# Kernel optimization log

Measured on AMD Instinct MI355X. Metric: run time of the kernel, lower is better.

Reference implementation:

```python
import jax, jax.numpy as jnp
import numpy as np

B, C, H, W = 4, 512, 32, 32
NUM_HEADS, DIM_HEAD = 16, 32
DIM_ATTN = NUM_HEADS * DIM_HEAD  # 512
N = H * W


def setup_inputs() -> dict:
    key = jax.random.key(0)
    ks = jax.random.split(key, 6)
    s = 0.02
    return {
        "x": jax.random.normal(ks[0], (B, C, H, W), jnp.float32),
        "w_qkv": jax.random.normal(ks[1], (3 * DIM_ATTN, C), jnp.float32) * s,
        "b_qkv": jax.random.normal(ks[2], (3 * DIM_ATTN,), jnp.float32) * s,
        "w_proj": jax.random.normal(ks[3], (C, DIM_ATTN), jnp.float32) * s,
        "b_proj": jax.random.normal(ks[4], (C,), jnp.float32) * s,
        "shared_rel_pos": jax.random.normal(ks[5], (1, NUM_HEADS, N, N), jnp.float32) * s,
    }


def reference(x, w_qkv, b_qkv, w_proj, b_proj, shared_rel_pos):
    b, c, h, w = x.shape
    n = h * w
    scale = DIM_HEAD ** -0.5
    # 1x1 conv == per-pixel matmul over channels
    qkv = jnp.einsum('bchw,oc->bohw', x, w_qkv) + b_qkv[None, :, None, None]
    # [B, heads, 3*dh, N] -> chunk along dim 2 (matches torch .chunk(3, dim=2))
    qkv = qkv.reshape(b, NUM_HEADS, 3 * DIM_HEAD, n)
    q, k, v = jnp.split(qkv, 3, axis=2)          # each [B, heads, dh, N]
    attn = jnp.einsum('bhdi,bhdj->bhij', q, k) * scale  # q^T @ k
    attn = attn + shared_rel_pos
    attn = jax.nn.softmax(attn, axis=-1)
    out = jnp.einsum('bhdj,bhij->bhdi', v, attn)  # v @ attn^T, [B, heads, dh, N]
    out = out.reshape(b, NUM_HEADS * DIM_HEAD, h, w)
    out = jnp.einsum('bchw,oc->bohw', out, w_proj) + b_proj[None, :, None, None]
    return out
```

## Files before the change

kernel.cpp:

```cpp
#include <hip/hip_runtime.h>
#include <cstdint>
#include <cstddef>

#define BATCH 4
#define CIN   512
#define NPIX  1024
#define HEADS 16
#define DH    32
#define DATTN 512
#define O_QKV 1536

typedef unsigned short u16;
typedef __bf16 bf16x4 __attribute__((ext_vector_type(4)));
typedef __bf16 bf16x8 __attribute__((ext_vector_type(8)));
typedef float  f32x4  __attribute__((ext_vector_type(4)));

typedef const __attribute__((address_space(1))) void g1_t;
typedef __attribute__((address_space(3))) void l3_t;

#if defined(__has_builtin)
#if __has_builtin(__builtin_amdgcn_exp2f)
#define EXP2(x) __builtin_amdgcn_exp2f(x)
#endif
#endif
#ifndef EXP2
#define EXP2(x) __expf((x) * 0.6931471805599453f)
#endif

__device__ __forceinline__ u16 f2bf(float f) {
  unsigned u = __float_as_uint(f);
  u += 0x7fffu + ((u >> 16) & 1u);
  return (u16)(u >> 16);
}

__device__ __forceinline__ void gl_lds16(const void* gp, void* lp) {
  __builtin_amdgcn_global_load_lds((g1_t*)gp, (l3_t*)lp, 16, 0, 0);
}

__global__ __launch_bounds__(256) void prep_w(const float* __restrict__ w1,
                                              const float* __restrict__ w2,
                                              u16* __restrict__ o1,
                                              u16* __restrict__ o2) {
  const int idx = blockIdx.x * 256 + threadIdx.x;
  const int n1 = (O_QKV * CIN) >> 2;
  float4 v = (idx < n1) ? reinterpret_cast<const float4*>(w1)[idx]
                        : reinterpret_cast<const float4*>(w2)[idx - n1];
  uint2 pk = make_uint2((unsigned)f2bf(v.x) | ((unsigned)f2bf(v.y) << 16),
                        (unsigned)f2bf(v.z) | ((unsigned)f2bf(v.w) << 16));
  if (idx < n1) reinterpret_cast<uint2*>(o1)[idx] = pk;
  else          reinterpret_cast<uint2*>(o2)[idx - n1] = pk;
}

__global__ __launch_bounds__(256) void prep_x(const float* __restrict__ x,
                                              u16* __restrict__ xt) {
  __shared__ float sT[64][65];
  const int t  = threadIdx.x;
  const int n0 = blockIdx.x * 64;
  const int c0 = blockIdx.y * 64;
  const int b  = blockIdx.z;
  const float* xb = x + ((size_t)b * CIN + c0) * NPIX + n0;
#pragma unroll
  for (int i = 0; i < 4; ++i) {
    int r   = i * 16 + (t >> 4);
    int col = (t & 15) << 2;
    float4 v = *reinterpret_cast<const float4*>(&xb[(size_t)r * NPIX + col]);
    sT[r][col + 0] = v.x; sT[r][col + 1] = v.y;
    sT[r][col + 2] = v.z; sT[r][col + 3] = v.w;
  }
  __syncthreads();
#pragma unroll
  for (int i = 0; i < 2; ++i) {
    int nl = t >> 2;
    int ch = (t & 3) + (i << 2);
    u16 tmp[8];
#pragma unroll
    for (int e = 0; e < 8; ++e) tmp[e] = f2bf(sT[(ch << 3) + e][nl]);
    *reinterpret_cast<uint4*>(&xt[((size_t)b * NPIX + n0 + nl) * CIN + c0 + (ch << 3)]) =
        *reinterpret_cast<uint4*>(tmp);
  }
}

__global__ __launch_bounds__(256) void gemm_qkv_mfma(const u16* __restrict__ wq,
                                                     const u16* __restrict__ xt,
                                                     const float* __restrict__ bias,
                                                     u16* __restrict__ qt,
                                                     u16* __restrict__ kt,
                                                     u16* __restrict__ vt) {
  __shared__ __align__(16) u16 sA[96 * 64];
  __shared__ __align__(16) u16 sB[128 * 64];
  const int t  = threadIdx.x;
  const int w  = t >> 6, l = t & 63, g = l >> 4, ln = l & 15;
  const int n0 = blockIdx.x * 128;
  const int h  = blockIdx.y;
  const int b  = blockIdx.z;
  const int wm = w >> 1, wn = w & 1;

  const u16* wbase = wq + (size_t)h * 96 * CIN;
  const u16* xbase = xt + ((size_t)b * NPIX + n0) * CIN;

  f32x4 acc[3][4];
#pragma unroll
  for (int mi = 0; mi < 3; ++mi)
#pragma unroll
    for (int ni = 0; ni < 4; ++ni) acc[mi][ni] = {0.f, 0.f, 0.f, 0.f};

  for (int k0 = 0; k0 < CIN; k0 += 64) {
#pragma unroll
    for (int i = 0; i < 3; ++i) {
      int chunk = i * 256 + (w << 6) + l;
      gl_lds16(wbase + ((size_t)(chunk >> 3)) * CIN + k0 + ((chunk & 7) << 3),
               (char*)sA + i * 4096 + (w << 10));
    }
#pragma unroll
    for (int i = 0; i < 4; ++i) {
      int chunk = i * 256 + (w << 6) + l;
      gl_lds16(xbase + ((size_t)(chunk >> 3)) * CIN + k0 + ((chunk & 7) << 3),
               (char*)sB + i * 4096 + (w << 10));
    }
    __syncthreads();
#pragma unroll
    for (int kk = 0; kk < 64; kk += 32) {
      bf16x8 af[3], bfr[4];
#pragma unroll
      for (int mi = 0; mi < 3; ++mi)
        af[mi] = *reinterpret_cast<const bf16x8*>(&sA[(48 * wm + 16 * mi + ln) * 64 + kk + (g << 3)]);
#pragma unroll
      for (int ni = 0; ni < 4; ++ni)
        bfr[ni] = *reinterpret_cast<const bf16x8*>(&sB[((wn << 6) + (ni << 4) + ln) * 64 + kk + (g << 3)]);
#pragma unroll
      for (int mi = 0; mi < 3; ++mi)
#pragma unroll
        for (int ni = 0; ni < 4; ++ni)
          acc[mi][ni] = __builtin_amdgcn_mfma_f32_16x16x32_bf16(af[mi], bfr[ni], acc[mi][ni], 0, 0, 0);
    }
    __syncthreads();
  }

  const float QSC = 0.17677669529663687f * 1.4426950408889634f;
  const float* bh = bias + h * 96;
#pragma unroll
  for (int mi = 0; mi < 3; ++mi) {
    const int sec = 48 * wm + 16 * mi;
    const int rb  = sec + (g << 2);
    const float b0 = bh[rb + 0], b1 = bh[rb + 1], b2 = bh[rb + 2], b3 = bh[rb + 3];
#pragma unroll
    for (int ni = 0; ni < 4; ++ni) {
      const int n = n0 + (wn << 6) + (ni << 4) + ln;
      f32x4 a = acc[mi][ni];
      float v0 = a[0] + b0, v1 = a[1] + b1, v2 = a[2] + b2, v3 = a[3] + b3;
      if (sec < 32) { v0 *= QSC; v1 *= QSC; v2 *= QSC; v3 *= QSC; }
      u16 e0 = f2bf(v0), e1 = f2bf(v1), e2 = f2bf(v2), e3 = f2bf(v3);
      if (sec < 32) {
        const int d = sec + (g << 2);
        uint2 pk = make_uint2((unsigned)e0 | ((unsigned)e1 << 16),
                              (unsigned)e2 | ((unsigned)e3 << 16));
        *reinterpret_cast<uint2*>(&qt[(((size_t)(b * HEADS + h)) * NPIX + n) * DH + d]) = pk;
      } else if (sec < 64) {
        const int d = sec - 32 + (g << 2);
        uint2 pk = make_uint2((unsigned)e0 | ((unsigned)e1 << 16),
                              (unsigned)e2 | ((unsigned)e3 << 16));
        *reinterpret_cast<uint2*>(&kt[(((size_t)(b * HEADS + h)) * NPIX + n) * DH + d]) = pk;
      } else {
        const int d = sec - 64 + (g << 2);
        u16* vp = &vt[(((size_t)(b * HEADS + h)) * DH + d) * NPIX + n];
        vp[0] = e0; vp[NPIX] = e1; vp[2 * NPIX] = e2; vp[3 * NPIX] = e3;
      }
    }
  }
}

__global__ __launch_bounds__(512, 4) void attn_mfma(const u16* __restrict__ qt,
                                                    const u16* __restrict__ kt,
                                                    const u16* __restrict__ vt,
                                                    const float* __restrict__ rel,
                                                    u16* __restrict__ aout) {
  __shared__ __align__(16) u16 sK[2][2][2048];
  __shared__ __align__(16) u16 sV[2][2][2048];
  __shared__ __align__(16) u16 sP[8][1024];

  const int t  = threadIdx.x;
  const int w  = t >> 6, l = t & 63, g = l >> 4, ln = l & 15;
  const int bid = blockIdx.x;
  const int xcd = bid & 7, sl = bid >> 3;
  const int b   = sl & 3;
  const int i0  = ((sl >> 2) & 15) << 6;
  const int h   = (xcd << 1) | (sl >> 6);
  const int iw  = w & 3;
  const int jh  = w >> 2;

  const size_t bh = (size_t)(b * HEADS + h);

  const int lr = l >> 3, ls = l & 7;
  const int sjh = w >> 2;
  const int kcl = ls ^ lr ^ (iw & 1);
  const int kj  = (iw << 4) + (lr << 1) + (kcl >> 2);
  const u16* ksrc = kt + (bh * NPIX + (sjh << 9) + kj) * DH + ((kcl & 3) << 3);
  const int vcl = ls ^ lr;
  const int vd  = (iw << 3) + lr;
  const u16* vsrc = vt + (bh * DH + vd) * NPIX + (sjh << 9) + (vcl << 3);
  char* kdst = (char*)&sK[0][sjh][0] + (iw << 10);
  char* vdst = (char*)&sV[0][sjh][0] + (iw << 10);

#define STAGE(s_, p_) do {                                          \
    gl_lds16(ksrc + (size_t)(s_) * 2048, kdst + (p_) * 8192);       \
    gl_lds16(vsrc + (size_t)(s_) * 64,   vdst + (p_) * 8192);       \
  } while (0)

  STAGE(0, 0);

  bf16x8 qf = *reinterpret_cast<const bf16x8*>(
      qt + (bh * NPIX + i0 + (iw << 4) + ln) * DH + (g << 3));

  const float* relp = rel + ((size_t)h * NPIX + i0 + (iw << 4) + (g << 2)) * NPIX +
                      (jh << 9) + (ln << 2);
  f32x4 relA4[4], relB4[4];
#pragma unroll
  for (int v = 0; v < 4; ++v)
    relA4[v] = *reinterpret_cast<const f32x4*>(relp + (size_t)v * NPIX);

  f32x4 vzero = {0.f, 0.f, 0.f, 0.f};
  f32x4 accO[2] = {vzero, vzero};
  f32x4 l_lane = vzero;

  u16* sPw = &sP[w][0];
  const float LOG2E = 1.4426950408889634f;

  for (int s = 0; s < 8; ++s) {
    const int p = s & 1;
    __syncthreads();
    if (s < 7) {
      STAGE(s + 1, p ^ 1);
#pragma unroll
      for (int v = 0; v < 4; ++v)
        relB4[v] = *reinterpret_cast<const f32x4*>(relp + (size_t)v * NPIX + ((s + 1) << 6));
    }

    const u16* Kb = &sK[p][jh][0];
    const u16* Vb = &sV[p][jh][0];

    f32x4 sfr[4];
    __builtin_amdgcn_s_setprio(1);
#pragma unroll
    for (int jj = 0; jj < 4; ++jj) {
      const int r  = (ln << 1) + (jj >> 1);
      const int ks = ((((jj & 1) << 2) | g) ^ (r & 7)) ^ ((r >> 3) & 1);
      bf16x8 kf = *reinterpret_cast<const bf16x8*>(Kb + r * 64 + ks * 8);
      sfr[jj] = __builtin_amdgcn_mfma_f32_16x16x32_bf16(qf, kf, vzero, 0, 0, 0);
    }
    __builtin_amdgcn_s_setprio(0);

#pragma unroll
    for (int v = 0; v < 4; ++v) {
      float p0 = EXP2(fmaf(relA4[v][0], LOG2E, sfr[0][v]));
      float p1 = EXP2(fmaf(relA4[v][1], LOG2E, sfr[1][v]));
      float p2 = EXP2(fmaf(relA4[v][2], LOG2E, sfr[2][v]));
      float p3 = EXP2(fmaf(relA4[v][3], LOG2E, sfr[3][v]));
      l_lane[v] += (p0 + p1) + (p2 + p3);
      bf16x4 pk;
      pk[0] = (__bf16)p0; pk[1] = (__bf16)p1; pk[2] = (__bf16)p2; pk[3] = (__bf16)p3;
      const int rw = (g << 2) + v;
      *reinterpret_cast<bf16x4*>(
          sPw + rw * 64 + ((((ln >> 1) ^ (rw & 7)) << 3) | ((ln & 1) << 2))) = pk;
    }

    __builtin_amdgcn_s_setprio(1);
#pragma unroll
    for (int kc = 0; kc < 2; ++kc) {
      const int lc = (kc << 2) | g;
      bf16x8 pa = *reinterpret_cast<const bf16x8*>(sPw + ln * 64 + ((lc ^ (ln & 7)) << 3));
#pragma unroll
      for (int dc = 0; dc < 2; ++dc) {
        const int d  = (dc << 4) + ln;
        const int vs = lc ^ (d & 7);
        bf16x8 vf = *reinterpret_cast<const bf16x8*>(Vb + d * 64 + vs * 8);
        accO[dc] = __builtin_amdgcn_mfma_f32_16x16x32_bf16(pa, vf, accO[dc], 0, 0, 0);
      }
    }
    __builtin_amdgcn_s_setprio(0);

    if (s < 7) {
#pragma unroll
      for (int v = 0; v < 4; ++v) relA4[v] = relB4[v];
    }
  }
#undef STAGE

  __syncthreads();
  float* mrg = (float*)&sK[0][0][0];
  if (jh == 1) {
    float* mp = mrg + ((size_t)((iw << 6) + l)) * 12;
    *reinterpret_cast<f32x4*>(mp + 0) = accO[0];
    *reinterpret_cast<f32x4*>(mp + 4) = accO[1];
    *reinterpret_cast<f32x4*>(mp + 8) = l_lane;
  }
  __syncthreads();
  if (jh == 0) {
    const float* mp = mrg + ((size_t)((iw << 6) + l)) * 12;
    f32x4 o0 = accO[0] + *reinterpret_cast<const f32x4*>(mp + 0);
    f32x4 o1 = accO[1] + *reinterpret_cast<const f32x4*>(mp + 4);
    f32x4 lv = l_lane + *reinterpret_cast<const f32x4*>(mp + 8);
#pragma unroll
    for (int v = 0; v < 4; ++v) {
      float ls2 = lv[v];
      ls2 += __shfl_xor(ls2, 1);
      ls2 += __shfl_xor(ls2, 2);
      ls2 += __shfl_xor(ls2, 4);
      ls2 += __shfl_xor(ls2, 8);
      const float inv = 1.f / ls2;
      const size_t row = (size_t)b * NPIX + i0 + (iw << 4) + (g << 2) + v;
      aout[row * DATTN + (h << 5) + ln]      = f2bf(o0[v] * inv);
      aout[row * DATTN + (h << 5) + 16 + ln] = f2bf(o1[v] * inv);
    }
  }
}

__global__ __launch_bounds__(256) void gemm_proj_mfma(const u16* __restrict__ wp,
                                                      const u16* __restrict__ at,
                                                      const float* __restrict__ bias,
                                                      float* __restrict__ out) {
  __shared__ __align__(16) u16 sA[64 * 64];
  __shared__ __align__(16) u16 sB[128 * 64];
  const int t  = threadIdx.x;
  const int w  = t >> 6, l = t & 63, g = l >> 4, ln = l & 15;
  const int n0 = blockIdx.x * 128;
  const int o0 = blockIdx.y * 64;
  const int b  = blockIdx.z;
  const int wm = w >> 1, wn = w & 1;

  const u16* wbase = wp + (size_t)o0 * DATTN;
  const u16* abase = at + ((size_t)b * NPIX + n0) * DATTN;

  f32x4 acc[2][4];
#pragma unroll
  for (int mi = 0; mi < 2; ++mi)
#pragma unroll
    for (int ni = 0; ni < 4; ++ni) acc[mi][ni] = {0.f, 0.f, 0.f, 0.f};

  for (int k0 = 0; k0 < DATTN; k0 += 64) {
#pragma unroll
    for (int i = 0; i < 2; ++i) {
      int chunk = i * 256 + (w << 6) + l;
      gl_lds16(wbase + ((size_t)(chunk >> 3)) * DATTN + k0 + ((chunk & 7) << 3),
               (char*)sA + i * 4096 + (w << 10));
    }
#pragma unroll
    for (int i = 0; i < 4; ++i) {
      int chunk = i * 256 + (w << 6) + l;
      gl_lds16(abase + ((size_t)(chunk >> 3)) * DATTN + k0 + ((chunk & 7) << 3),
               (char*)sB + i * 4096 + (w << 10));
    }
    __syncthreads();
#pragma unroll
    for (int kk = 0; kk < 64; kk += 32) {
      bf16x8 af[2], bfr[4];
#pragma unroll
      for (int mi = 0; mi < 2; ++mi)
        af[mi] = *reinterpret_cast<const bf16x8*>(&sA[((wm << 5) + (mi << 4) + ln) * 64 + kk + (g << 3)]);
#pragma unroll
      for (int ni = 0; ni < 4; ++ni)
        bfr[ni] = *reinterpret_cast<const bf16x8*>(&sB[((wn << 6) + (ni << 4) + ln) * 64 + kk + (g << 3)]);
#pragma unroll
      for (int mi = 0; mi < 2; ++mi)
#pragma unroll
        for (int ni = 0; ni < 4; ++ni)
          acc[mi][ni] = __builtin_amdgcn_mfma_f32_16x16x32_bf16(af[mi], bfr[ni], acc[mi][ni], 0, 0, 0);
    }
    __syncthreads();
  }

#pragma unroll
  for (int mi = 0; mi < 2; ++mi) {
    const int o = o0 + (wm << 5) + (mi << 4) + (g << 2);
    const float b0 = bias[o], b1 = bias[o + 1], b2 = bias[o + 2], b3 = bias[o + 3];
#pragma unroll
    for (int ni = 0; ni < 4; ++ni) {
      const int n = n0 + (wn << 6) + (ni << 4) + ln;
      float* op = &out[((size_t)b * DATTN + o) * NPIX + n];
      op[0]        = acc[mi][ni][0] + b0;
      op[NPIX]     = acc[mi][ni][1] + b1;
      op[2 * NPIX] = acc[mi][ni][2] + b2;
      op[3 * NPIX] = acc[mi][ni][3] + b3;
    }
  }
}

extern "C" void kernel_launch(void* const* d_in, const int* in_sizes, int n_in,
                              void* d_out, int out_size, void* d_ws, size_t ws_size,
                              hipStream_t stream) {
  (void)in_sizes; (void)n_in; (void)out_size; (void)ws_size;
  const float* x      = (const float*)d_in[0];
  const float* w_qkv  = (const float*)d_in[1];
  const float* b_qkv  = (const float*)d_in[2];
  const float* w_proj = (const float*)d_in[3];
  const float* b_proj = (const float*)d_in[4];
  const float* rel    = (const float*)d_in[5];
  float* out = (float*)d_out;

  u16* xt    = (u16*)d_ws;
  u16* wq_bf = xt + (size_t)BATCH * NPIX * CIN;
  u16* wp_bf = wq_bf + (size_t)O_QKV * CIN;
  u16* qt    = wp_bf + (size_t)DATTN * DATTN;
  u16* kt    = qt + (size_t)BATCH * HEADS * NPIX * DH;
  u16* vt    = kt + (size_t)BATCH * HEADS * NPIX * DH;
  u16* aout  = vt + (size_t)BATCH * HEADS * NPIX * DH;

  prep_w<<<1024, 256, 0, stream>>>(w_qkv, w_proj, wq_bf, wp_bf);
  prep_x<<<dim3(NPIX / 64, CIN / 64, BATCH), 256, 0, stream>>>(x, xt);
  gemm_qkv_mfma<<<dim3(NPIX / 128, HEADS, BATCH), 256, 0, stream>>>(wq_bf, xt, b_qkv, qt, kt, vt);
  attn_mfma<<<1024, 512, 0, stream>>>(qt, kt, vt, rel, aout);
  gemm_proj_mfma<<<dim3(NPIX / 128, DATTN / 64, BATCH), 256, 0, stream>>>(wp_bf, aout, b_proj, out);
}
```

Before: 63.61 us.

## Software-pipeline PV MFMA one stage behind QK in attention loop

Defers the P·V MFMA of each stage to the start of the next loop iteration, preloading the V fragments into registers at the end of each iteration and draining the last stage after the loop. The aim is to let the PV matrix work overlap with the next stage's global staging and the QK MFMA/exp work instead of serialising behind the softmax LDS writes. It also precomputes the swizzled LDS offsets once. The cost is extra live registers for four bf16x8 V fragments, which could lower occupancy. The sP reads now happen after the next __syncthreads, which still looks ordered correctly because each wave owns its own sP slice.

```diff
diff --git a/kernel.cpp b/kernel.cpp
--- a/kernel.cpp
+++ b/kernel.cpp
@@ -222,8 +222,17 @@
   f32x4 accO[2] = {vzero, vzero};
   f32x4 l_lane = vzero;
 
+  bf16x8 vf00, vf01, vf10, vf11;
+
   u16* sPw = &sP[w][0];
   const float LOG2E = 1.4426950408889634f;
+
+  const int paOff0 = ln * 64 + ((g ^ (ln & 7)) << 3);
+  const int paOff1 = ln * 64 + (((4 | g) ^ (ln & 7)) << 3);
+  const int vOff00 = ln * 64 + ((g ^ (ln & 7)) << 3);
+  const int vOff01 = (16 + ln) * 64 + ((g ^ ((16 + ln) & 7)) << 3);
+  const int vOff10 = ln * 64 + (((4 | g) ^ (ln & 7)) << 3);
+  const int vOff11 = (16 + ln) * 64 + (((4 | g) ^ ((16 + ln) & 7)) << 3);
 
   for (int s = 0; s < 8; ++s) {
     const int p = s & 1;
@@ -233,6 +242,17 @@
 #pragma unroll
       for (int v = 0; v < 4; ++v)
         relB4[v] = *reinterpret_cast<const f32x4*>(relp + (size_t)v * NPIX + ((s + 1) << 6));
+    }
+
+    if (s > 0) {
+      __builtin_amdgcn_s_setprio(1);
+      bf16x8 pa0 = *reinterpret_cast<const bf16x8*>(sPw + paOff0);
+      accO[0] = __builtin_amdgcn_mfma_f32_16x16x32_bf16(pa0, vf00, accO[0], 0, 0, 0);
+      accO[1] = __builtin_amdgcn_mfma_f32_16x16x32_bf16(pa0, vf01, accO[1], 0, 0, 0);
+      bf16x8 pa1 = *reinterpret_cast<const bf16x8*>(sPw + paOff1);
+      accO[0] = __builtin_amdgcn_mfma_f32_16x16x32_bf16(pa1, vf10, accO[0], 0, 0, 0);
+      accO[1] = __builtin_amdgcn_mfma_f32_16x16x32_bf16(pa1, vf11, accO[1], 0, 0, 0);
+      __builtin_amdgcn_s_setprio(0);
     }
 
     const u16* Kb = &sK[p][jh][0];
@@ -263,27 +283,28 @@
           sPw + rw * 64 + ((((ln >> 1) ^ (rw & 7)) << 3) | ((ln & 1) << 2))) = pk;
     }
 
+    vf00 = *reinterpret_cast<const bf16x8*>(Vb + vOff00);
+    vf01 = *reinterpret_cast<const bf16x8*>(Vb + vOff01);
+    vf10 = *reinterpret_cast<const bf16x8*>(Vb + vOff10);
+    vf11 = *reinterpret_cast<const bf16x8*>(Vb + vOff11);
+
+    if (s < 7) {
+#pragma unroll
+      for (int v = 0; v < 4; ++v) relA4[v] = relB4[v];
+    }
+  }
+#undef STAGE
+
+  {
     __builtin_amdgcn_s_setprio(1);
-#pragma unroll
-    for (int kc = 0; kc < 2; ++kc) {
-      const int lc = (kc << 2) | g;
-      bf16x8 pa = *reinterpret_cast<const bf16x8*>(sPw + ln * 64 + ((lc ^ (ln & 7)) << 3));
-#pragma unroll
-      for (int dc = 0; dc < 2; ++dc) {
-        const int d  = (dc << 4) + ln;
-        const int vs = lc ^ (d & 7);
-        bf16x8 vf = *reinterpret_cast<const bf16x8*>(Vb + d * 64 + vs * 8);
-        accO[dc] = __builtin_amdgcn_mfma_f32_16x16x32_bf16(pa, vf, accO[dc], 0, 0, 0);
-      }
-    }
+    bf16x8 pa0 = *reinterpret_cast<const bf16x8*>(sPw + paOff0);
+    accO[0] = __builtin_amdgcn_mfma_f32_16x16x32_bf16(pa0, vf00, accO[0], 0, 0, 0);
+    accO[1] = __builtin_amdgcn_mfma_f32_16x16x32_bf16(pa0, vf01, accO[1], 0, 0, 0);
+    bf16x8 pa1 = *reinterpret_cast<const bf16x8*>(sPw + paOff1);
+    accO[0] = __builtin_amdgcn_mfma_f32_16x16x32_bf16(pa1, vf10, accO[0], 0, 0, 0);
+    accO[1] = __builtin_amdgcn_mfma_f32_16x16x32_bf16(pa1, vf11, accO[1], 0, 0, 0);
     __builtin_amdgcn_s_setprio(0);
-
-    if (s < 7) {
-#pragma unroll
-      for (int v = 0; v < 4; ++v) relA4[v] = relB4[v];
-    }
-  }
-#undef STAGE
+  }
 
   __syncthreads();
   float* mrg = (float*)&sK[0][0][0];
```

New measurement: 63.13 us. About the same (-0.8%).

## Halve attention block to 4 waves, each processing two 16-row query tiles

Applied to the files above, without the earlier changes.

The attention kernel now launches 256 threads per block instead of 512. Each wave handles two 16-row query fragments, so every K and V fragment read from LDS feeds two MFMAs. Each thread issues twice as many global-to-LDS staging loads per stage. The register double-buffering of rel_pos is dropped: rel values are loaded each iteration right before use. This trades fewer waves per block and less latency hiding on the rel loads for more register reuse of K/V and fewer LDS reads per MFMA.

```diff
diff --git a/kernel.cpp b/kernel.cpp
--- a/kernel.cpp
+++ b/kernel.cpp
@@ -169,14 +169,14 @@
   }
 }
 
-__global__ __launch_bounds__(512, 4) void attn_mfma(const u16* __restrict__ qt,
+__global__ __launch_bounds__(256, 3) void attn_mfma(const u16* __restrict__ qt,
                                                     const u16* __restrict__ kt,
                                                     const u16* __restrict__ vt,
                                                     const float* __restrict__ rel,
                                                     u16* __restrict__ aout) {
   __shared__ __align__(16) u16 sK[2][2][2048];
   __shared__ __align__(16) u16 sV[2][2][2048];
-  __shared__ __align__(16) u16 sP[8][1024];
+  __shared__ __align__(16) u16 sP[4][2048];
 
   const int t  = threadIdx.x;
   const int w  = t >> 6, l = t & 63, g = l >> 4, ln = l & 15;
@@ -185,42 +185,52 @@
   const int b   = sl & 3;
   const int i0  = ((sl >> 2) & 15) << 6;
   const int h   = (xcd << 1) | (sl >> 6);
-  const int iw  = w & 3;
-  const int jh  = w >> 2;
+  const int iw2 = w & 1;
+  const int jh  = w >> 1;
 
   const size_t bh = (size_t)(b * HEADS + h);
 
-  const int lr = l >> 3, ls = l & 7;
-  const int sjh = w >> 2;
-  const int kcl = ls ^ lr ^ (iw & 1);
-  const int kj  = (iw << 4) + (lr << 1) + (kcl >> 2);
-  const u16* ksrc = kt + (bh * NPIX + (sjh << 9) + kj) * DH + ((kcl & 3) << 3);
-  const int vcl = ls ^ lr;
-  const int vd  = (iw << 3) + lr;
-  const u16* vsrc = vt + (bh * DH + vd) * NPIX + (sjh << 9) + (vcl << 3);
-  char* kdst = (char*)&sK[0][sjh][0] + (iw << 10);
-  char* vdst = (char*)&sV[0][sjh][0] + (iw << 10);
-
-#define STAGE(s_, p_) do {                                          \
-    gl_lds16(ksrc + (size_t)(s_) * 2048, kdst + (p_) * 8192);       \
-    gl_lds16(vsrc + (size_t)(s_) * 64,   vdst + (p_) * 8192);       \
+  const int hs = w & 1;
+  const int c0 = (hs << 7) + l;
+  const int r0 = c0 >> 3,      s0 = c0 & 7;
+  const int c1 = c0 + 64;
+  const int r1 = c1 >> 3,      s1 = c1 & 7;
+  const int kc0 = s0 ^ (r0 & 7) ^ ((r0 >> 3) & 1);
+  const int kc1 = s1 ^ (r1 & 7) ^ ((r1 >> 3) & 1);
+  const int vc0 = s0 ^ (r0 & 7);
+  const int vc1 = s1 ^ (r1 & 7);
+  const u16* ksrc0 = kt + (bh * NPIX + (jh << 9) + ((r0 << 1) | (kc0 >> 2))) * DH + ((kc0 & 3) << 3);
+  const u16* ksrc1 = kt + (bh * NPIX + (jh << 9) + ((r1 << 1) | (kc1 >> 2))) * DH + ((kc1 & 3) << 3);
+  const u16* vsrc0 = vt + (bh * DH + r0) * NPIX + (jh << 9) + (vc0 << 3);
+  const u16* vsrc1 = vt + (bh * DH + r1) * NPIX + (jh << 9) + (vc1 << 3);
+  char* kdst = (char*)&sK[0][jh][0] + (hs << 11);
+  char* vdst = (char*)&sV[0][jh][0] + (hs << 11);
+
+#define STAGE(s_, p_) do {                                            \
+    gl_lds16(ksrc0 + (size_t)(s_) * 2048, kdst + (p_) * 8192);        \
+    gl_lds16(ksrc1 + (size_t)(s_) * 2048, kdst + (p_) * 8192 + 1024); \
+    gl_lds16(vsrc0 + (size_t)(s_) * 64,   vdst + (p_) * 8192);        \
+    gl_lds16(vsrc1 + (size_t)(s_) * 64,   vdst + (p_) * 8192 + 1024); \
   } while (0)
 
   STAGE(0, 0);
 
-  bf16x8 qf = *reinterpret_cast<const bf16x8*>(
-      qt + (bh * NPIX + i0 + (iw << 4) + ln) * DH + (g << 3));
-
-  const float* relp = rel + ((size_t)h * NPIX + i0 + (iw << 4) + (g << 2)) * NPIX +
+  bf16x8 qf[2];
+#pragma unroll
+  for (int f = 0; f < 2; ++f)
+    qf[f] = *reinterpret_cast<const bf16x8*>(
+        qt + (bh * NPIX + i0 + (iw2 << 5) + (f << 4) + ln) * DH + (g << 3));
+
+  const float* relp = rel + ((size_t)h * NPIX + i0 + (iw2 << 5) + (g << 2)) * NPIX +
                       (jh << 9) + (ln << 2);
-  f32x4 relA4[4], relB4[4];
-#pragma unroll
-  for (int v = 0; v < 4; ++v)
-    relA4[v] = *reinterpret_cast<const f32x4*>(relp + (size_t)v * NPIX);
 
   f32x4 vzero = {0.f, 0.f, 0.f, 0.f};
-  f32x4 accO[2] = {vzero, vzero};
-  f32x4 l_lane = vzero;
+  f32x4 accO[2][2];
+  f32x4 l_lane[2];
+#pragma unroll
+  for (int f = 0; f < 2; ++f) {
+    accO[f][0] = vzero; accO[f][1] = vzero; l_lane[f] = vzero;
+  }
 
   u16* sPw = &sP[w][0];
   const float LOG2E = 1.4426950408889634f;
@@ -228,88 +238,103 @@
   for (int s = 0; s < 8; ++s) {
     const int p = s & 1;
     __syncthreads();
-    if (s < 7) {
-      STAGE(s + 1, p ^ 1);
+    if (s < 7) STAGE(s + 1, p ^ 1);
+
+    f32x4 relv[2][4];
+#pragma unroll
+    for (int f = 0; f < 2; ++f)
 #pragma unroll
       for (int v = 0; v < 4; ++v)
-        relB4[v] = *reinterpret_cast<const f32x4*>(relp + (size_t)v * NPIX + ((s + 1) << 6));
-    }
+        relv[f][v] = *reinterpret_cast<const f32x4*>(
+            relp + ((size_t)((f << 4) + v)) * NPIX + (s << 6));
 
     const u16* Kb = &sK[p][jh][0];
     const u16* Vb = &sV[p][jh][0];
 
-    f32x4 sfr[4];
+    f32x4 sfr[2][4];
     __builtin_amdgcn_s_setprio(1);
 #pragma unroll
     for (int jj = 0; jj < 4; ++jj) {
       const int r  = (ln << 1) + (jj >> 1);
       const int ks = ((((jj & 1) << 2) | g) ^ (r & 7)) ^ ((r >> 3) & 1);
       bf16x8 kf = *reinterpret_cast<const bf16x8*>(Kb + r * 64 + ks * 8);
-      sfr[jj] = __builtin_amdgcn_mfma_f32_16x16x32_bf16(qf, kf, vzero, 0, 0, 0);
+      sfr[0][jj] = __builtin_amdgcn_mfma_f32_16x16x32_bf16(qf[0], kf, vzero, 0, 0, 0);
+      sfr[1][jj] = __builtin_amdgcn_mfma_f32_16x16x32_bf16(qf[1], kf, vzero, 0, 0, 0);
     }
     __builtin_amdgcn_s_setprio(0);
 
 #pragma unroll
-    for (int v = 0; v < 4; ++v) {
-      float p0 = EXP2(fmaf(relA4[v][0], LOG2E, sfr[0][v]));
-      float p1 = EXP2(fmaf(relA4[v][1], LOG2E, sfr[1][v]));
-      float p2 = EXP2(fmaf(relA4[v][2], LOG2E, sfr[2][v]));
-      float p3 = EXP2(fmaf(relA4[v][3], LOG2E, sfr[3][v]));
-      l_lane[v] += (p0 + p1) + (p2 + p3);
-      bf16x4 pk;
-      pk[0] = (__bf16)p0; pk[1] = (__bf16)p1; pk[2] = (__bf16)p2; pk[3] = (__bf16)p3;
-      const int rw = (g << 2) + v;
-      *reinterpret_cast<bf16x4*>(
-          sPw + rw * 64 + ((((ln >> 1) ^ (rw & 7)) << 3) | ((ln & 1) << 2))) = pk;
+    for (int f = 0; f < 2; ++f) {
+      u16* sPf = sPw + (f << 10);
+#pragma unroll
+      for (int v = 0; v < 4; ++v) {
+        float p0 = EXP2(fmaf(relv[f][v][0], LOG2E, sfr[f][0][v]));
+        float p1 = EXP2(fmaf(relv[f][v][1], LOG2E, sfr[f][1][v]));
+        float p2 = EXP2(fmaf(relv[f][v][2], LOG2E, sfr[f][2][v]));
+        float p3 = EXP2(fmaf(relv[f][v][3], LOG2E, sfr[f][3][v]));
+        l_lane[f][v] += (p0 + p1) + (p2 + p3);
+        bf16x4 pk;
+        pk[0] = (__bf16)p0; pk[1] = (__bf16)p1; pk[2] = (__bf16)p2; pk[3] = (__bf16)p3;
+        const int rw = (g << 2) + v;
+        *reinterpret_cast<bf16x4*>(
+            sPf + rw * 64 + ((((ln >> 1) ^ (rw & 7)) << 3) | ((ln & 1) << 2))) = pk;
+      }
     }
 
     __builtin_amdgcn_s_setprio(1);
 #pragma unroll
     for (int kc = 0; kc < 2; ++kc) {
       const int lc = (kc << 2) | g;
-      bf16x8 pa = *reinterpret_cast<const bf16x8*>(sPw + ln * 64 + ((lc ^ (ln & 7)) << 3));
-#pragma unroll
-      for (int dc = 0; dc < 2; ++dc) {
-        const int d  = (dc << 4) + ln;
-        const int vs = lc ^ (d & 7);
-        bf16x8 vf = *reinterpret_cast<const bf16x8*>(Vb + d * 64 + vs * 8);
-        accO[dc] = __builtin_amdgcn_mfma_f32_16x16x32_bf16(pa, vf, accO[dc], 0, 0, 0);
+      bf16x8 vf0, vf1;
+      {
+        const int d0 = ln;
+        const int d1 = 16 + ln;
+        vf0 = *reinterpret_cast<const bf16x8*>(Vb + d0 * 64 + ((lc ^ (d0 & 7)) << 3));
+        vf1 = *reinterpret_cast<const bf16x8*>(Vb + d1 * 64 + ((lc ^ (d1 & 7)) << 3));
       }
+#pragma unroll
+      for (int f = 0; f < 2; ++f) {
+        bf16x8 pa = *reinterpret_cast<const bf16x8*>(
+            sPw + (f << 10) + ln * 64 + ((lc ^ (ln & 7)) << 3));
+        accO[f][0] = __builtin_amdgcn_mfma_f32_16x16x32_bf16(pa, vf0, accO[f][0], 0, 0, 0);
+        accO[f][1] = __builtin_amdgcn_mfma_f32_16x16x32_bf16(pa, vf1, accO[f][1], 0, 0, 0);
+      }
     }
     __builtin_amdgcn_s_setprio(0);
-
-    if (s < 7) {
-#pragma unroll
-      for (int v = 0; v < 4; ++v) relA4[v] = relB4[v];
-    }
   }
 #undef STAGE
 
   __syncthreads();
   float* mrg = (float*)&sK[0][0][0];
   if (jh == 1) {
-    float* mp = mrg + ((size_t)((iw << 6) + l)) * 12;
-    *reinterpret_cast<f32x4*>(mp + 0) = accO[0];
-    *reinterpret_cast<f32x4*>(mp + 4) = accO[1];
-    *reinterpret_cast<f32x4*>(mp + 8) = l_lane;
+#pragma unroll
+    for (int f = 0; f < 2; ++f) {
+      float* mp = mrg + ((size_t)(((iw2 << 1) + f) << 6) + l) * 12;
+      *reinterpret_cast<f32x4*>(mp + 0) = accO[f][0];
+      *reinterpret_cast<f32x4*>(mp + 4) = accO[f][1];
+      *reinterpret_cast<f32x4*>(mp + 8) = l_lane[f];
+    }
   }
   __syncthreads();
   if (jh == 0) {
-    const float* mp = mrg + ((size_t)((iw << 6) + l)) * 12;
-    f32x4 o0 = accO[0] + *reinterpret_cast<const f32x4*>(mp + 0);
-    f32x4 o1 = accO[1] + *reinterpret_cast<const f32x4*>(mp + 4);
-    f32x4 lv = l_lane + *reinterpret_cast<const f32x4*>(mp + 8);
-#pragma unroll
-    for (int v = 0; v < 4; ++v) {
-      float ls2 = lv[v];
-      ls2 += __shfl_xor(ls2, 1);
-      ls2 += __shfl_xor(ls2, 2);
-      ls2 += __shfl_xor(ls2, 4);
-      ls2 += __shfl_xor(ls2, 8);
-      const float inv = 1.f / ls2;
-      const size_t row = (size_t)b * NPIX + i0 + (iw << 4) + (g << 2) + v;
-      aout[row * DATTN + (h << 5) + ln]      = f2bf(o0[v] * inv);
-      aout[row * DATTN + (h << 5) + 16 + ln] = f2bf(o1[v] * inv);
+#pragma unroll
+    for (int f = 0; f < 2; ++f) {
+      const float* mp = mrg + ((size_t)(((iw2 << 1) + f) << 6) + l) * 12;
+      f32x4 o0 = accO[f][0] + *reinterpret_cast<const f32x4*>(mp + 0);
+      f32x4 o1 = accO[f][1] + *reinterpret_cast<const f32x4*>(mp + 4);
+      f32x4 lv = l_lane[f] + *reinterpret_cast<const f32x4*>(mp + 8);
+#pragma unroll
+      for (int v = 0; v < 4; ++v) {
+        float ls2 = lv[v];
+        ls2 += __shfl_xor(ls2, 1);
+        ls2 += __shfl_xor(ls2, 2);
+        ls2 += __shfl_xor(ls2, 4);
+        ls2 += __shfl_xor(ls2, 8);
+        const float inv = 1.f / ls2;
+        const size_t row = (size_t)b * NPIX + i0 + (iw2 << 5) + (f << 4) + (g << 2) + v;
+        aout[row * DATTN + (h << 5) + ln]      = f2bf(o0[v] * inv);
+        aout[row * DATTN + (h << 5) + 16 + ln] = f2bf(o1[v] * inv);
+      }
     }
   }
 }
@@ -407,6 +432,6 @@
   prep_w<<<1024, 256, 0, stream>>>(w_qkv, w_proj, wq_bf, wp_bf);
   prep_x<<<dim3(NPIX / 64, CIN / 64, BATCH), 256, 0, stream>>>(x, xt);
   gemm_qkv_mfma<<<dim3(NPIX / 128, HEADS, BATCH), 256, 0, stream>>>(wq_bf, xt, b_qkv, qt, kt, vt);
-  attn_mfma<<<1024, 512, 0, stream>>>(qt, kt, vt, rel, aout);
+  attn_mfma<<<1024, 256, 0, stream>>>(qt, kt, vt, rel, aout);
   gemm_proj_mfma<<<dim3(NPIX / 128, DATTN / 64, BATCH), 256, 0, stream>>>(wp_bf, aout, b_proj, out);
 }
```

After: 70.33 us. +10.6%, slower.

## Compute transposed scores so P stays in registers, dropping LDS round-trip

Applied to the files above, without the earlier changes.

The QK^T MFMA now takes its operands in swapped order, so each lane holds score values already laid out as the A-operand of the PV MFMA. The probabilities are packed directly into bf16x8 registers instead of being written to and reread from a per-wave shared-memory buffer, which removes the sP array and its LDS traffic. K and V LDS offsets are precomputed outside the loop, and the rel-pos bias is loaded per step with a new column-major mapping instead of being double-buffered in registers. Row sums are reduced across lanes with a different shuffle pattern. The risk is that rel loads are no longer prefetched a step ahead, which can expose global-memory latency.

```diff
diff --git a/kernel.cpp b/kernel.cpp
--- a/kernel.cpp
+++ b/kernel.cpp
@@ -176,7 +176,6 @@
                                                     u16* __restrict__ aout) {
   __shared__ __align__(16) u16 sK[2][2][2048];
   __shared__ __align__(16) u16 sV[2][2][2048];
-  __shared__ __align__(16) u16 sP[8][1024];
 
   const int t  = threadIdx.x;
   const int w  = t >> 6, l = t & 63, g = l >> 4, ln = l & 15;
@@ -211,29 +210,42 @@
   bf16x8 qf = *reinterpret_cast<const bf16x8*>(
       qt + (bh * NPIX + i0 + (iw << 4) + ln) * DH + (g << 3));
 
-  const float* relp = rel + ((size_t)h * NPIX + i0 + (iw << 4) + (g << 2)) * NPIX +
-                      (jh << 9) + (ln << 2);
-  f32x4 relA4[4], relB4[4];
-#pragma unroll
-  for (int v = 0; v < 4; ++v)
-    relA4[v] = *reinterpret_cast<const f32x4*>(relp + (size_t)v * NPIX);
+  int kOff[4];
+#pragma unroll
+  for (int jj = 0; jj < 4; ++jj) {
+    const int j = ((jj >> 1) << 5) + ((ln >> 2) << 3) + ((jj & 1) << 2) + (ln & 3);
+    const int r = j >> 1;
+    const int c = ((j & 1) << 2) | g;
+    const int slot = (c ^ (r & 7)) ^ ((r >> 3) & 1);
+    kOff[jj] = r * 64 + slot * 8;
+  }
+  int vOff[2][2];
+#pragma unroll
+  for (int kc = 0; kc < 2; ++kc)
+#pragma unroll
+    for (int dc = 0; dc < 2; ++dc) {
+      const int d = (dc << 4) + ln;
+      vOff[kc][dc] = d * 64 + ((((kc << 2) | g) ^ (d & 7)) << 3);
+    }
+
+  const float* relp = rel + ((size_t)h * NPIX + i0 + (iw << 4) + ln) * NPIX +
+                      (jh << 9) + (g << 3);
 
   f32x4 vzero = {0.f, 0.f, 0.f, 0.f};
   f32x4 accO[2] = {vzero, vzero};
-  f32x4 l_lane = vzero;
-
-  u16* sPw = &sP[w][0];
+  float l_part = 0.f;
+
   const float LOG2E = 1.4426950408889634f;
 
   for (int s = 0; s < 8; ++s) {
     const int p = s & 1;
     __syncthreads();
-    if (s < 7) {
-      STAGE(s + 1, p ^ 1);
-#pragma unroll
-      for (int v = 0; v < 4; ++v)
-        relB4[v] = *reinterpret_cast<const f32x4*>(relp + (size_t)v * NPIX + ((s + 1) << 6));
-    }
+    if (s < 7) STAGE(s + 1, p ^ 1);
+
+    f32x4 r00 = *reinterpret_cast<const f32x4*>(relp + (s << 6));
+    f32x4 r01 = *reinterpret_cast<const f32x4*>(relp + (s << 6) + 4);
+    f32x4 r10 = *reinterpret_cast<const f32x4*>(relp + (s << 6) + 32);
+    f32x4 r11 = *reinterpret_cast<const f32x4*>(relp + (s << 6) + 36);
 
     const u16* Kb = &sK[p][jh][0];
     const u16* Vb = &sV[p][jh][0];
@@ -242,48 +254,42 @@
     __builtin_amdgcn_s_setprio(1);
 #pragma unroll
     for (int jj = 0; jj < 4; ++jj) {
-      const int r  = (ln << 1) + (jj >> 1);
-      const int ks = ((((jj & 1) << 2) | g) ^ (r & 7)) ^ ((r >> 3) & 1);
-      bf16x8 kf = *reinterpret_cast<const bf16x8*>(Kb + r * 64 + ks * 8);
-      sfr[jj] = __builtin_amdgcn_mfma_f32_16x16x32_bf16(qf, kf, vzero, 0, 0, 0);
+      bf16x8 kf = *reinterpret_cast<const bf16x8*>(Kb + kOff[jj]);
+      sfr[jj] = __builtin_amdgcn_mfma_f32_16x16x32_bf16(kf, qf, vzero, 0, 0, 0);
     }
     __builtin_amdgcn_s_setprio(0);
 
+    bf16x8 pa0, pa1;
 #pragma unroll
     for (int v = 0; v < 4; ++v) {
-      float p0 = EXP2(fmaf(relA4[v][0], LOG2E, sfr[0][v]));
-      float p1 = EXP2(fmaf(relA4[v][1], LOG2E, sfr[1][v]));
-      float p2 = EXP2(fmaf(relA4[v][2], LOG2E, sfr[2][v]));
-      float p3 = EXP2(fmaf(relA4[v][3], LOG2E, sfr[3][v]));
-      l_lane[v] += (p0 + p1) + (p2 + p3);
-      bf16x4 pk;
-      pk[0] = (__bf16)p0; pk[1] = (__bf16)p1; pk[2] = (__bf16)p2; pk[3] = (__bf16)p3;
-      const int rw = (g << 2) + v;
-      *reinterpret_cast<bf16x4*>(
-          sPw + rw * 64 + ((((ln >> 1) ^ (rw & 7)) << 3) | ((ln & 1) << 2))) = pk;
+      float p0 = EXP2(fmaf(r00[v], LOG2E, sfr[0][v]));
+      float p1 = EXP2(fmaf(r01[v], LOG2E, sfr[1][v]));
+      float p2 = EXP2(fmaf(r10[v], LOG2E, sfr[2][v]));
+      float p3 = EXP2(fmaf(r11[v], LOG2E, sfr[3][v]));
+      l_part += (p0 + p1) + (p2 + p3);
+      pa0[v]     = (__bf16)p0;
+      pa0[4 + v] = (__bf16)p1;
+      pa1[v]     = (__bf16)p2;
+      pa1[4 + v] = (__bf16)p3;
     }
 
     __builtin_amdgcn_s_setprio(1);
-#pragma unroll
-    for (int kc = 0; kc < 2; ++kc) {
-      const int lc = (kc << 2) | g;
-      bf16x8 pa = *reinterpret_cast<const bf16x8*>(sPw + ln * 64 + ((lc ^ (ln & 7)) << 3));
-#pragma unroll
-      for (int dc = 0; dc < 2; ++dc) {
-        const int d  = (dc << 4) + ln;
-        const int vs = lc ^ (d & 7);
-        bf16x8 vf = *reinterpret_cast<const bf16x8*>(Vb + d * 64 + vs * 8);
-        accO[dc] = __builtin_amdgcn_mfma_f32_16x16x32_bf16(pa, vf, accO[dc], 0, 0, 0);
-      }
+    {
+      bf16x8 vf00 = *reinterpret_cast<const bf16x8*>(Vb + vOff[0][0]);
+      bf16x8 vf01 = *reinterpret_cast<const bf16x8*>(Vb + vOff[0][1]);
+      accO[0] = __builtin_amdgcn_mfma_f32_16x16x32_bf16(pa0, vf00, accO[0], 0, 0, 0);
+      accO[1] = __builtin_amdgcn_mfma_f32_16x16x32_bf16(pa0, vf01, accO[1], 0, 0, 0);
+      bf16x8 vf10 = *reinterpret_cast<const bf16x8*>(Vb + vOff[1][0]);
+      bf16x8 vf11 = *reinterpret_cast<const bf16x8*>(Vb + vOff[1][1]);
+      accO[0] = __builtin_amdgcn_mfma_f32_16x16x32_bf16(pa1, vf10, accO[0], 0, 0, 0);
+      accO[1] = __builtin_amdgcn_mfma_f32_16x16x32_bf16(pa1, vf11, accO[1], 0, 0, 0);
     }
     __builtin_amdgcn_s_setprio(0);
-
-    if (s < 7) {
-#pragma unroll
-      for (int v = 0; v < 4; ++v) relA4[v] = relB4[v];
-    }
   }
 #undef STAGE
+
+  l_part += __shfl_xor(l_part, 16);
+  l_part += __shfl_xor(l_part, 32);
 
   __syncthreads();
   float* mrg = (float*)&sK[0][0][0];
@@ -291,22 +297,18 @@
     float* mp = mrg + ((size_t)((iw << 6) + l)) * 12;
     *reinterpret_cast<f32x4*>(mp + 0) = accO[0];
     *reinterpret_cast<f32x4*>(mp + 4) = accO[1];
-    *reinterpret_cast<f32x4*>(mp + 8) = l_lane;
+    mp[8] = l_part;
   }
   __syncthreads();
   if (jh == 0) {
     const float* mp = mrg + ((size_t)((iw << 6) + l)) * 12;
     f32x4 o0 = accO[0] + *reinterpret_cast<const f32x4*>(mp + 0);
     f32x4 o1 = accO[1] + *reinterpret_cast<const f32x4*>(mp + 4);
-    f32x4 lv = l_lane + *reinterpret_cast<const f32x4*>(mp + 8);
+    float lsum = l_part + mp[8];
 #pragma unroll
     for (int v = 0; v < 4; ++v) {
-      float ls2 = lv[v];
-      ls2 += __shfl_xor(ls2, 1);
-      ls2 += __shfl_xor(ls2, 2);
-      ls2 += __shfl_xor(ls2, 4);
-      ls2 += __shfl_xor(ls2, 8);
-      const float inv = 1.f / ls2;
+      const float lrow = __shfl(lsum, (g << 2) + v);
+      const float inv = 1.f / lrow;
       const size_t row = (size_t)b * NPIX + i0 + (iw << 4) + (g << 2) + v;
       aout[row * DATTN + (h << 5) + ln]      = f2bf(o0[v] * inv);
       aout[row * DATTN + (h << 5) + 16 + ln] = f2bf(o1[v] * inv);
```

Result: slower. 76.15 us (+19.7%).
